# Optimization experiments

Hardware: AMD Instinct MI355X
Metric: run time of the kernel (lower is better)

## Reference

```python
import jax, jax.numpy as jnp
import numpy as np

P, D, C, F, B = 8, 2, 64, 64, 2048  # properties, disjuncts/property, classes, features, batch
T = P * D


def _make_post_graphs():
    # Each disjunct is a sparse DAG over classes: edge (i, j) means y_i >= y_j required.
    rng = np.random.RandomState(0)
    g = (rng.rand(T, C, C) < 0.05).astype(np.int32)
    return jnp.asarray(np.triu(g, k=1))


def setup_inputs():
    key = jax.random.key(0)
    kx, ky = jax.random.split(key)
    return {
        "x": jax.random.normal(kx, (B, F), jnp.float32),
        "y": jax.random.normal(ky, (B, C), jnp.float32),
        "post_graphs": _make_post_graphs(),
    }


def _contains_cycle(graph):
    # Kahn peel: repeatedly delete in-degree-0 nodes; cycle iff nodes remain. graph: [B,C,C]
    gf = graph.astype(jnp.float32)
    def body(_, rem):
        indeg = jnp.einsum('bi,bij->bj', rem, gf)
        return jnp.where((rem > 0) & (indeg == 0), 0.0, rem)
    rem = jax.lax.fori_loop(0, C, body, jnp.ones(graph.shape[:2], jnp.float32))
    return jnp.any(rem > 0, axis=1)


def _topo_ranks(y, graph):
    # Priority topological sort: among in-degree-0 remaining nodes pick max-y first.
    # rank[b, c] = position of class c in the topological order.
    gf = graph.astype(jnp.float32)
    n = y.shape[0]
    rows = jnp.arange(n)
    def step(carry, r):
        rem, rank = carry
        indeg = jnp.einsum('bi,bij->bj', rem, gf)
        score = jnp.where((rem > 0) & (indeg == 0), y, -jnp.inf)
        idx = jnp.argmax(score, axis=1)
        rank = rank.at[rows, idx].set(r)
        rem = rem * (1.0 - jax.nn.one_hot(idx, C, dtype=jnp.float32))
        return (rem, rank), None
    init = (jnp.ones((n, C), jnp.float32), jnp.zeros((n, C), jnp.int32))
    (_, rank), _ = jax.lax.scan(step, init, jnp.arange(C))
    return rank


def _forward(x, y, post_graphs):
    n = y.shape[0]
    required = (x[:, :P] > 0.0).astype(jnp.int32)          # [B,P] precondition satisfaction
    # 'preserve' heuristic: order disjuncts by ascending violation of current y
    diff = jax.nn.relu(y[:, None, :] - y[:, :, None])       # [B,C,C] relu(y_j - y_i)
    viol = jnp.einsum('bij,tij->bt', diff, post_graphs.astype(jnp.float32)).reshape(n, P, D)
    order = jnp.argsort(jax.lax.stop_gradient(viol), axis=2)  # [B,P,D]
    # greedy disjunction solve: per property, first heuristic-ordered choice whose union is acyclic
    acc = jnp.zeros((n, C, C), jnp.int32)
    for p in range(P):
        cand = post_graphs[p * D:(p + 1) * D]               # [D,C,C]
        chosen = order[:, p, 0]
        found = jnp.zeros((n,), bool)
        for k in range(D):
            dk = order[:, p, k]
            test = jnp.maximum(acc, required[:, p, None, None] * cand[dk])
            ok = ~_contains_cycle(test)
            chosen = jnp.where(found, chosen, jnp.where(ok, dk, chosen))
            found = found | ok
        acc = jnp.maximum(acc, required[:, p, None, None] * cand[chosen])  # graph_union
    graph = acc                                              # [B,C,C] selected postcondition graph
    rank = _topo_ranks(jax.lax.stop_gradient(y), graph)
    y_desc = -jnp.sort(-y, axis=1)                           # descending values of y
    y_fixed = jnp.take_along_axis(y_desc, rank, axis=1)      # assign sorted values by topo order
    sat = jnp.all((graph == 0) | (y[:, :, None] >= y[:, None, :]), axis=(1, 2))
    y_rep = jnp.where(sat[:, None], y, y_fixed)              # keep y where already satisfied
    gb = graph > 0
    margin = jnp.sum(jnp.where(gb, jax.nn.relu(y_rep[:, None, :] - y_rep[:, :, None]), 0.0), axis=(1, 2))
    bot = jnp.where(margin > 0.0, jnp.max(y_rep, axis=1) + margin, -jnp.inf)
    return jnp.concatenate([y_rep, bot[:, None]], axis=1)    # [B, C+1]


def reference(x, y, post_graphs):
    return _forward(x, y, post_graphs)
```

## Files before the change

### kernel.cpp

```cpp
#include <hip/hip_runtime.h>
#include <hip/hip_bf16.h>
#include <float.h>


#define C_NODES 64
#define T_GRAPHS 16
#define P_PHASES 8
#define F_DIM 64
#define MAXE 160
#define KITER (MAXE / 4)

typedef unsigned long long u64;

__device__ __forceinline__ float finite_or_zero(float v) {
    unsigned u = __float_as_uint(v);
    return ((u & 0x7f800000u) == 0x7f800000u) ? 0.0f : v;
}

__global__ __launch_bounds__(64) void gor_prep_v9(
    const int* __restrict__ g, u64* __restrict__ maskT,
    unsigned short* __restrict__ elist) {
    const int t = blockIdx.x;
    const int lane = threadIdx.x;

    const uint4* row = (const uint4*)(g + (t * C_NODES + lane) * C_NODES);
    u64 m = 0ull;
    #pragma unroll
    for (int q = 0; q < 16; ++q) {
        uint4 v = row[q];
        m |= ((u64)(v.x != 0u)) << (4 * q + 0);
        m |= ((u64)(v.y != 0u)) << (4 * q + 1);
        m |= ((u64)(v.z != 0u)) << (4 * q + 2);
        m |= ((u64)(v.w != 0u)) << (4 * q + 3);
    }

    u64 mt = 0ull;
    #pragma unroll
    for (int j = 0; j < C_NODES; ++j) {
        u64 cm = __ballot((m >> j) & 1ull);
        if (j == lane) mt = cm;
    }
    maskT[t * C_NODES + lane] = mt;

    int cnt = __popcll(m);
    int incl = cnt;
    #pragma unroll
    for (int off = 1; off < 64; off <<= 1) {
        int v = __shfl_up(incl, off);
        if (lane >= off) incl += v;
    }
    const int excl = incl - cnt;
    const int tot = __shfl(incl, 63);

    u64 mm = m;
    int e = excl;
    while (mm) {
        int j = __builtin_ctzll(mm); mm &= mm - 1;
        if (e < MAXE)
            elist[(e >> 2) * 64 + 16 * (e & 3) + t] =
                (unsigned short)((lane << 8) | j);
        ++e;
    }
    for (int e2 = tot + lane; e2 < MAXE; e2 += 64)
        elist[(e2 >> 2) * 64 + 16 * (e2 & 3) + t] = 0;
}

__global__ __launch_bounds__(64) void gor_repair_v9(
    const float* __restrict__ x, const float* __restrict__ y,
    const u64* __restrict__ maskT, const unsigned short* __restrict__ elist,
    float* __restrict__ out) {
    const int b = blockIdx.x;
    const int lane = threadIdx.x;

    __shared__ float y_s[C_NODES];
    __shared__ int perm_s[C_NODES];

    const float y_l = finite_or_zero(y[b * C_NODES + lane]);
    y_s[lane] = y_l;
    __syncthreads();

    const u64 req = __ballot((lane < P_PHASES) && (x[b * F_DIM + lane] > 0.0f));

    float vp = 0.0f;
    #pragma unroll
    for (int k = 0; k < KITER; ++k) {
        unsigned ev = elist[k * 64 + lane];
        float yi = y_s[ev >> 8];
        float yj = y_s[ev & 255u];
        float d = yj - yi;
        vp += (d > 0.0f) ? d : 0.0f;
    }
    vp += __shfl_xor(vp, 16);
    vp += __shfl_xor(vp, 32);

    const int p8 = lane & 7;
    const float va = __shfl(vp, 2 * p8);
    const float vb = __shfl(vp, 2 * p8 + 1);
    const u64 takeb = __ballot((lane < P_PHASES) && (vb < va));

    const float minv = ((takeb >> p8) & 1ull) ? vb : va;
    const bool myok =
        (lane >= P_PHASES) || !((req >> p8) & 1ull) || (minv == 0.0f);
    const bool sat = (__all((int)myok) != 0);

    if (sat) {
        out[b * (C_NODES + 1) + lane] = y_l;
    } else {
        int dpos = 0;
        #pragma unroll
        for (int j = 0; j < C_NODES; ++j) {
            float yj = y_s[j];
            dpos += (yj > y_l) || (yj == y_l && j < lane);
        }
        perm_s[dpos] = lane;
        __syncthreads();

        const int n = perm_s[lane];

        u64 predcol = 0ull;
        #pragma unroll
        for (int p = 0; p < P_PHASES; ++p) {
            if ((req >> p) & 1ull) {
                const int tsel = 2 * p + (int)((takeb >> p) & 1ull);
                predcol |= maskT[tsel * C_NODES + lane];
            }
        }
        unsigned plo = (unsigned)__shfl((int)(unsigned)predcol, n);
        unsigned phi = (unsigned)__shfl((int)(unsigned)(predcol >> 32), n);
        const u64 pred_n = ((u64)phi << 32) | (u64)plo;

        const float y_slot = __shfl(y_l, n);

        u64 remN = ~0ull;
        bool my_rem = true;
        int myrank = 0;
        for (int r = 0; r < C_NODES; ++r) {
            bool avail = my_rem && ((pred_n & remN) == 0ull);
            u64 bb = __ballot(avail);
            int d = __builtin_ctzll(bb);
            if (d == lane) myrank = r;
            my_rem = my_rem && (d != lane);
            int nch = __shfl(n, d);
            remN &= ~(1ull << nch);
        }

        out[b * (C_NODES + 1) + n] = __shfl(y_slot, myrank);
    }

    if (lane == 0) out[b * (C_NODES + 1) + C_NODES] = 0.0f;
}

extern "C" void kernel_launch(void* const* d_in, const int* in_sizes, int n_in,
                              void* d_out, int out_size, void* d_ws, size_t ws_size,
                              hipStream_t stream) {
    const float* x = (const float*)d_in[0];
    const float* y = (const float*)d_in[1];
    const int* post_graphs = (const int*)d_in[2];
    float* out = (float*)d_out;

    const int B = in_sizes[1] / C_NODES;

    u64* maskT = (u64*)d_ws;
    unsigned short* elist = (unsigned short*)((char*)d_ws + 8192);

    gor_prep_v9<<<T_GRAPHS, C_NODES, 0, stream>>>(post_graphs, maskT, elist);
    gor_repair_v9<<<B, C_NODES, 0, stream>>>(x, y, maskT, elist, out);
}
```

Baseline: 20.58 us.

## Replace shared memory with lane shuffles and packed edge-list loads in repair kernel

Removes the shared-memory staging of y and the permutation buffer in the repair kernel. Values now move through wave shuffles, readlane and ds_permute, so both __syncthreads barriers are gone. Edge pairs are packed into 32-bit words and preloaded into registers, and the mask transpose in the prep kernel becomes a 6-level butterfly shuffle instead of 64 ballots. The catch is that each edge now costs two shuffles instead of LDS reads, and register pressure goes up from the 20 preloaded words.

```diff
diff --git a/kernel.cpp b/kernel.cpp
--- a/kernel.cpp
+++ b/kernel.cpp
@@ -8,7 +8,7 @@
 #define P_PHASES 8
 #define F_DIM 64
 #define MAXE 160
-#define KITER (MAXE / 4)
+#define K2 20
 
 typedef unsigned long long u64;
 
@@ -16,10 +16,16 @@
     unsigned u = __float_as_uint(v);
     return ((u & 0x7f800000u) == 0x7f800000u) ? 0.0f : v;
 }
+__device__ __forceinline__ int rl_i(int v, int l) {
+    return __builtin_amdgcn_readlane(v, l);
+}
+__device__ __forceinline__ float rl_f(float v, int l) {
+    return __int_as_float(__builtin_amdgcn_readlane(__float_as_int(v), l));
+}
 
-__global__ __launch_bounds__(64) void gor_prep_v9(
+__global__ __launch_bounds__(64) void gor_prep_v10(
     const int* __restrict__ g, u64* __restrict__ maskT,
-    unsigned short* __restrict__ elist) {
+    unsigned short* __restrict__ elist16) {
     const int t = blockIdx.x;
     const int lane = threadIdx.x;
 
@@ -34,11 +40,19 @@
         m |= ((u64)(v.w != 0u)) << (4 * q + 3);
     }
 
-    u64 mt = 0ull;
+    u64 mt = m;
+    const u64 AM[6] = {0x5555555555555555ull, 0x3333333333333333ull,
+                       0x0F0F0F0F0F0F0F0Full, 0x00FF00FF00FF00FFull,
+                       0x0000FFFF0000FFFFull, 0x00000000FFFFFFFFull};
     #pragma unroll
-    for (int j = 0; j < C_NODES; ++j) {
-        u64 cm = __ballot((m >> j) & 1ull);
-        if (j == lane) mt = cm;
+    for (int lev = 0; lev < 6; ++lev) {
+        const int j = 1 << lev;
+        unsigned lo = (unsigned)__shfl_xor((int)(unsigned)mt, j);
+        unsigned hi = (unsigned)__shfl_xor((int)(unsigned)(mt >> 32), j);
+        u64 part = ((u64)hi << 32) | (u64)lo;
+        const u64 A = AM[lev];
+        mt = ((lane & j) == 0) ? ((mt & A) | ((part & A) << j))
+                               : ((mt & ~A) | ((part & ~A) >> j));
     }
     maskT[t * C_NODES + lane] = mt;
 
@@ -50,45 +64,49 @@
         if (lane >= off) incl += v;
     }
     const int excl = incl - cnt;
-    const int tot = __shfl(incl, 63);
+    const int tot = __builtin_amdgcn_readfirstlane(__shfl(incl, 63));
 
     u64 mm = m;
     int e = excl;
     while (mm) {
         int j = __builtin_ctzll(mm); mm &= mm - 1;
-        if (e < MAXE)
-            elist[(e >> 2) * 64 + 16 * (e & 3) + t] =
+        if (e < MAXE) {
+            int l = 16 * (e & 3) + t;
+            elist16[(((e >> 3) * 64 + l) << 1) + ((e >> 2) & 1)] =
                 (unsigned short)((lane << 8) | j);
+        }
         ++e;
     }
-    for (int e2 = tot + lane; e2 < MAXE; e2 += 64)
-        elist[(e2 >> 2) * 64 + 16 * (e2 & 3) + t] = 0;
+    for (int e2 = tot + lane; e2 < MAXE; e2 += 64) {
+        int l = 16 * (e2 & 3) + t;
+        elist16[(((e2 >> 3) * 64 + l) << 1) + ((e2 >> 2) & 1)] = 0;
+    }
 }
 
-__global__ __launch_bounds__(64) void gor_repair_v9(
+__global__ __launch_bounds__(64) void gor_repair_v10(
     const float* __restrict__ x, const float* __restrict__ y,
-    const u64* __restrict__ maskT, const unsigned short* __restrict__ elist,
+    const u64* __restrict__ maskT, const unsigned* __restrict__ elist32,
     float* __restrict__ out) {
     const int b = blockIdx.x;
     const int lane = threadIdx.x;
 
-    __shared__ float y_s[C_NODES];
-    __shared__ int perm_s[C_NODES];
+    const float y_l = finite_or_zero(y[b * C_NODES + lane]);
+    const u64 req = __ballot((lane < P_PHASES) && (x[b * F_DIM + lane] > 0.0f));
 
-    const float y_l = finite_or_zero(y[b * C_NODES + lane]);
-    y_s[lane] = y_l;
-    __syncthreads();
-
-    const u64 req = __ballot((lane < P_PHASES) && (x[b * F_DIM + lane] > 0.0f));
+    unsigned ereg[K2];
+    #pragma unroll
+    for (int k2 = 0; k2 < K2; ++k2) ereg[k2] = elist32[k2 * 64 + lane];
 
     float vp = 0.0f;
     #pragma unroll
-    for (int k = 0; k < KITER; ++k) {
-        unsigned ev = elist[k * 64 + lane];
-        float yi = y_s[ev >> 8];
-        float yj = y_s[ev & 255u];
-        float d = yj - yi;
-        vp += (d > 0.0f) ? d : 0.0f;
+    for (int k2 = 0; k2 < K2; ++k2) {
+        const unsigned w = ereg[k2];
+        const int i0 = (w >> 8) & 255, j0 = (int)(w & 255u);
+        const int i1 = (int)(w >> 24), j1 = (w >> 16) & 255;
+        float d0 = __shfl(y_l, j0) - __shfl(y_l, i0);
+        vp += (d0 > 0.0f) ? d0 : 0.0f;
+        float d1 = __shfl(y_l, j1) - __shfl(y_l, i1);
+        vp += (d1 > 0.0f) ? d1 : 0.0f;
     }
     vp += __shfl_xor(vp, 16);
     vp += __shfl_xor(vp, 32);
@@ -103,19 +121,16 @@
         (lane >= P_PHASES) || !((req >> p8) & 1ull) || (minv == 0.0f);
     const bool sat = (__all((int)myok) != 0);
 
+    float* orow = out + b * (C_NODES + 1);
     if (sat) {
-        out[b * (C_NODES + 1) + lane] = y_l;
+        orow[lane] = y_l;
     } else {
         int dpos = 0;
-        #pragma unroll
         for (int j = 0; j < C_NODES; ++j) {
-            float yj = y_s[j];
+            const float yj = rl_f(y_l, j);
             dpos += (yj > y_l) || (yj == y_l && j < lane);
         }
-        perm_s[dpos] = lane;
-        __syncthreads();
-
-        const int n = perm_s[lane];
+        const int n = __builtin_amdgcn_ds_permute(dpos << 2, lane);
 
         u64 predcol = 0ull;
         #pragma unroll
@@ -125,29 +140,29 @@
                 predcol |= maskT[tsel * C_NODES + lane];
             }
         }
-        unsigned plo = (unsigned)__shfl((int)(unsigned)predcol, n);
-        unsigned phi = (unsigned)__shfl((int)(unsigned)(predcol >> 32), n);
+        const unsigned plo = (unsigned)__shfl((int)(unsigned)predcol, n);
+        const unsigned phi = (unsigned)__shfl((int)(unsigned)(predcol >> 32), n);
         const u64 pred_n = ((u64)phi << 32) | (u64)plo;
-
         const float y_slot = __shfl(y_l, n);
 
         u64 remN = ~0ull;
         bool my_rem = true;
         int myrank = 0;
         for (int r = 0; r < C_NODES; ++r) {
-            bool avail = my_rem && ((pred_n & remN) == 0ull);
-            u64 bb = __ballot(avail);
-            int d = __builtin_ctzll(bb);
+            const bool avail = my_rem && ((pred_n & remN) == 0ull);
+            const u64 bb = __ballot(avail);
+            const int d =
+                __builtin_amdgcn_readfirstlane((int)__builtin_ctzll(bb));
             if (d == lane) myrank = r;
             my_rem = my_rem && (d != lane);
-            int nch = __shfl(n, d);
+            const int nch = rl_i(n, d);
             remN &= ~(1ull << nch);
         }
 
-        out[b * (C_NODES + 1) + n] = __shfl(y_slot, myrank);
+        orow[n] = __shfl(y_slot, myrank);
     }
 
-    if (lane == 0) out[b * (C_NODES + 1) + C_NODES] = 0.0f;
+    if (lane == 0) orow[C_NODES] = 0.0f;
 }
 
 extern "C" void kernel_launch(void* const* d_in, const int* in_sizes, int n_in,
@@ -161,8 +176,9 @@
     const int B = in_sizes[1] / C_NODES;
 
     u64* maskT = (u64*)d_ws;
-    unsigned short* elist = (unsigned short*)((char*)d_ws + 8192);
+    unsigned short* elist16 = (unsigned short*)((char*)d_ws + 8192);
+    const unsigned* elist32 = (const unsigned*)((char*)d_ws + 8192);
 
-    gor_prep_v9<<<T_GRAPHS, C_NODES, 0, stream>>>(post_graphs, maskT, elist);
-    gor_repair_v9<<<B, C_NODES, 0, stream>>>(x, y, maskT, elist, out);
+    gor_prep_v10<<<T_GRAPHS, C_NODES, 0, stream>>>(post_graphs, maskT, elist16);
+    gor_repair_v10<<<B, C_NODES, 0, stream>>>(x, y, maskT, elist32, out);
 }
```

New measurement: 20.57 us. About the same (-0.1%).
